# Performance work log

Hardware: AMD Instinct MI355X
Metric: run time of the kernel (lower is better)

The kernel has to match this reference:

```python
import jax, jax.numpy as jnp
import numpy as np
from jax import lax

ACT_BITS = 8
O, C, K = 256, 128, 3
STRIDE, PAD = 1, 1


def setup_inputs() -> dict:
    key = jax.random.key(0)
    kx, kw = jax.random.split(key)
    x = jax.random.uniform(kx, (16, C, 56, 56), dtype=jnp.float32)
    weight = jax.random.normal(kw, (O, C, K, K), dtype=jnp.float32)
    wrange = 2 ** 8  # weight_bits
    qw = jnp.clip(jnp.round(weight * (wrange - 1)), 0, wrange - 1)
    # PCILT: pcilt[o,c,kh,kw,i] = qw[o,c,kh,kw] * i  for i in [0, 2^act_bits)
    A = 2 ** ACT_BITS
    pcilt = qw[..., None] * jnp.arange(A, dtype=jnp.float32)  # [O,C,K,K,A]
    bias = jnp.zeros((O,), dtype=jnp.float32)
    return {"x": x, "pcilt": pcilt, "bias": bias}


def reference(x, pcilt, bias):
    A = pcilt.shape[-1]
    # quantize activations to integer LUT indices in [0, A-1]
    xq = jnp.clip(jnp.round(x * (A - 1)), 0.0, A - 1.0)
    # The gather-and-sum  out[b,o,h,w] = sum_{c,kh,kw} pcilt[o,c,kh,kw, idx]
    # is mathematically identical to a conv with qw = pcilt[...,1] applied to the
    # (float-cast) quantized indices, since pcilt[...,i] == qw * i exactly.
    qw = pcilt[..., 1]  # [O,C,K,K] quantized weights
    out = lax.conv_general_dilated(
        xq, qw,
        window_strides=(STRIDE, STRIDE),
        padding=((PAD, PAD), (PAD, PAD)),
        dimension_numbers=("NCHW", "OIHW", "NCHW"),
    )
    return out + bias[None, :, None, None]
```

## Files before the change

### kernel.cpp

```cpp
#include <hip/hip_runtime.h>
#include <stdint.h>

typedef unsigned short u16;
typedef __bf16 bf16x8 __attribute__((ext_vector_type(8)));
typedef float f32x4 __attribute__((ext_vector_type(4)));
typedef unsigned short u16x8 __attribute__((ext_vector_type(8)));

#define B_N   16
#define C_CH  128
#define O_CH  256
#define HW    56
#define PH    58
#define PW    72
#define PHW   (PH * PW)

__global__ void quant_pad(const float* __restrict__ x, u16* __restrict__ xp) {
    int idx = blockIdx.x * 256 + threadIdx.x;
    int wp = idx % PW;
    int hp = (idx / PW) % PH;
    int bc = idx / PHW;
    int h = hp - 1, w = wp - 1;
    u16 bits = 0;
    if ((unsigned)h < HW && (unsigned)w < HW) {
        float v = x[(bc * HW + h) * HW + w];
        float q = fminf(fmaxf(rintf(v * 255.0f), 0.0f), 255.0f);
        bits = (u16)(__float_as_uint(q) >> 16);
    }
    xp[idx] = bits;
}

__global__ void make_w(const float* __restrict__ pcilt, u16* __restrict__ Bq) {
    int idx = blockIdx.x * 256 + threadIdx.x;
    int o = idx % O_CH;
    int c = (idx / O_CH) % C_CH;
    int r = idx / (O_CH * C_CH);
    float v = pcilt[(size_t)(((o * C_CH + c) * 9 + r)) * 256 + 1];
    Bq[idx] = (u16)(__float_as_uint(v) >> 16);
}

__global__ __launch_bounds__(256) void conv_mfma(const u16* __restrict__ xp,
                                                 const u16* __restrict__ Bq,
                                                 const float* __restrict__ bias,
                                                 float* __restrict__ out) {
    __shared__ __align__(16) u16 Ws[4][128][8];
    __shared__ __align__(16) u16 Is[4][128][8];

    const int tid = threadIdx.x;
    const int o_blk = blockIdx.x * 128;
    const int h0 = blockIdx.y * 2;
    const int b = blockIdx.z;

    const int lane = tid & 63;
    const int wid = tid >> 6;
    const int wo = wid & 1;
    const int wm = wid >> 1;

    f32x4 acc[4][4];
#pragma unroll
    for (int i = 0; i < 4; i++)
#pragma unroll
        for (int j = 0; j < 4; j++) acc[i][j] = (f32x4){0.f, 0.f, 0.f, 0.f};

    const int sm = tid & 127;
    const int g0 = tid >> 7;
    const int sdh = sm >> 6;
    const int sw = sm & 63;

    const int quad = lane >> 4;
    const int lrow = lane & 15;

    for (int r = 0; r < 9; ++r) {
        const int kh = r / 3, kw = r % 3;
        const int xrow_base = (b * C_CH * PH + (h0 + sdh + kh)) * PW + (sw + kw);
        const int brow_base = r * C_CH * O_CH + (o_blk + sm);

        for (int cc = 0; cc < 4; ++cc) {
            const int c0 = cc * 32;
            __syncthreads();
#pragma unroll
            for (int gg = 0; gg < 2; ++gg) {
                const int g = g0 + gg * 2;
                u16x8 v;
#pragma unroll
                for (int e = 0; e < 8; ++e) {
                    const int c = c0 + g * 8 + e;
                    v[e] = xp[xrow_base + c * PHW];
                }
                *(u16x8*)&Is[g][sm][0] = v;
            }
#pragma unroll
            for (int gg = 0; gg < 2; ++gg) {
                const int g = g0 + gg * 2;
                u16x8 v;
#pragma unroll
                for (int e = 0; e < 8; ++e) {
                    const int c = c0 + g * 8 + e;
                    v[e] = Bq[brow_base + c * O_CH];
                }
                *(u16x8*)&Ws[g][sm][0] = v;
            }
            __syncthreads();
            bf16x8 af[4], bfr[4];
#pragma unroll
            for (int i = 0; i < 4; i++)
                af[i] = *(const bf16x8*)&Ws[quad][wo * 64 + i * 16 + lrow][0];
#pragma unroll
            for (int j = 0; j < 4; j++)
                bfr[j] = *(const bf16x8*)&Is[quad][wm * 64 + j * 16 + lrow][0];
#pragma unroll
            for (int i = 0; i < 4; i++)
#pragma unroll
                for (int j = 0; j < 4; j++)
                    acc[i][j] = __builtin_amdgcn_mfma_f32_16x16x32_bf16(af[i], bfr[j], acc[i][j], 0, 0, 0);
        }
    }

    const int hh = h0 + wm;
#pragma unroll
    for (int i = 0; i < 4; i++) {
        const int obase = o_blk + wo * 64 + i * 16 + quad * 4;
#pragma unroll
        for (int j = 0; j < 4; j++) {
            const int w = j * 16 + lrow;
            if (w < HW) {
#pragma unroll
                for (int rg = 0; rg < 4; ++rg) {
                    const int o = obase + rg;
                    out[(((size_t)b * O_CH + o) * HW + hh) * HW + w] = acc[i][j][rg] + bias[o];
                }
            }
        }
    }
}

extern "C" void kernel_launch(void* const* d_in, const int* in_sizes, int n_in,
                              void* d_out, int out_size, void* d_ws, size_t ws_size,
                              hipStream_t stream) {
    const float* x     = (const float*)d_in[0];
    const float* pcilt = (const float*)d_in[1];
    const float* bias  = (const float*)d_in[2];
    float* out = (float*)d_out;

    u16* xp = (u16*)d_ws;
    u16* Bq = xp + (size_t)B_N * C_CH * PHW;

    quant_pad<<<(B_N * C_CH * PHW) / 256, 256, 0, stream>>>(x, xp);
    make_w<<<(9 * C_CH * O_CH) / 256, 256, 0, stream>>>(pcilt, Bq);
    conv_mfma<<<dim3(O_CH / 128, HW / 2, B_N), dim3(256), 0, stream>>>(xp, Bq, bias, out);
}
```

Measured before the change: 453.5 us.

## Switch activations and weights to channel-last layout with direct global-to-LDS loads

The quantize/pad kernel now writes activations in NHWC order (channels innermost) through an LDS transpose, and the weight table is stored with input channel innermost. With contiguous channels, the conv kernel fills its LDS tiles with 16-byte global_load_lds transfers instead of eight strided 2-byte gathers per element. This removes uncoalesced scalar loads and register staging from the main loop. The cost is a more involved quantize kernel with a shared-memory transpose.

```diff
diff --git a/kernel.cpp b/kernel.cpp
--- a/kernel.cpp
+++ b/kernel.cpp
@@ -4,7 +4,6 @@
 typedef unsigned short u16;
 typedef __bf16 bf16x8 __attribute__((ext_vector_type(8)));
 typedef float f32x4 __attribute__((ext_vector_type(4)));
-typedef unsigned short u16x8 __attribute__((ext_vector_type(8)));
 
 #define B_N   16
 #define C_CH  128
@@ -12,28 +11,50 @@
 #define HW    56
 #define PH    58
 #define PW    72
-#define PHW   (PH * PW)
 
-__global__ void quant_pad(const float* __restrict__ x, u16* __restrict__ xp) {
-    int idx = blockIdx.x * 256 + threadIdx.x;
-    int wp = idx % PW;
-    int hp = (idx / PW) % PH;
-    int bc = idx / PHW;
-    int h = hp - 1, w = wp - 1;
-    u16 bits = 0;
-    if ((unsigned)h < HW && (unsigned)w < HW) {
-        float v = x[(bc * HW + h) * HW + w];
-        float q = fminf(fmaxf(rintf(v * 255.0f), 0.0f), 255.0f);
-        bits = (u16)(__float_as_uint(q) >> 16);
-    }
-    xp[idx] = bits;
+#define GLOBAL_AS __attribute__((address_space(1)))
+#define LDS_AS    __attribute__((address_space(3)))
+
+__device__ __forceinline__ void glds16(const u16* g, u16* l) {
+    __builtin_amdgcn_global_load_lds((const GLOBAL_AS void*)g, (LDS_AS void*)l, 16, 0, 0);
 }
 
-__global__ void make_w(const float* __restrict__ pcilt, u16* __restrict__ Bq) {
+__global__ __launch_bounds__(256) void quant_pad(const float* __restrict__ x,
+                                                 u16* __restrict__ xp) {
+    __shared__ u16 Lt[C_CH][58];
+    const int hp = blockIdx.x;
+    const int b = blockIdx.y;
+    const int tid = threadIdx.x;
+    const int h = hp - 1;
+    const bool interior = (unsigned)h < HW;
+
+    if (interior) {
+        for (int i = 0; i < 28; ++i) {
+            int idx = i * 256 + tid;
+            int c = idx / HW, w = idx % HW;
+            float v = x[((b * C_CH + c) * HW + h) * HW + w];
+            float q = fminf(fmaxf(rintf(v * 255.0f), 0.0f), 255.0f);
+            Lt[c][w] = (u16)(__float_as_uint(q) >> 16);
+        }
+    }
+    __syncthreads();
+    u16* dst = xp + ((size_t)(b * PH + hp) * PW) * C_CH;
+    for (int j = 0; j < 36; ++j) {
+        int idx = j * 256 + tid;
+        int wp = idx / C_CH, c = idx % C_CH;
+        int w = wp - 1;
+        u16 bits = 0;
+        if (interior && (unsigned)w < HW) bits = Lt[c][w];
+        dst[idx] = bits;
+    }
+}
+
+__global__ __launch_bounds__(256) void make_w(const float* __restrict__ pcilt,
+                                              u16* __restrict__ Bq) {
     int idx = blockIdx.x * 256 + threadIdx.x;
-    int o = idx % O_CH;
-    int c = (idx / O_CH) % C_CH;
-    int r = idx / (O_CH * C_CH);
+    int c = idx % C_CH;
+    int o = (idx / C_CH) % O_CH;
+    int r = idx / (C_CH * O_CH);
     float v = pcilt[(size_t)(((o * C_CH + c) * 9 + r)) * 256 + 1];
     Bq[idx] = (u16)(__float_as_uint(v) >> 16);
 }
@@ -61,45 +82,33 @@
 #pragma unroll
         for (int j = 0; j < 4; j++) acc[i][j] = (f32x4){0.f, 0.f, 0.f, 0.f};
 
-    const int sm = tid & 127;
-    const int g0 = tid >> 7;
-    const int sdh = sm >> 6;
-    const int sw = sm & 63;
+    const u16* pI0 = xp + ((size_t)(b * PH + h0) * PW + lane) * C_CH + wid * 8;
+    const u16* pI1 = pI0 + (size_t)PW * C_CH;
+    const u16* pW0 = Bq + (size_t)(o_blk + lane) * C_CH + wid * 8;
+    const u16* pW1 = pW0 + 64 * C_CH;
+    u16* lI0 = &Is[wid][0][0];
+    u16* lI1 = &Is[wid][64][0];
+    u16* lW0 = &Ws[wid][0][0];
+    u16* lW1 = &Ws[wid][64][0];
 
     const int quad = lane >> 4;
     const int lrow = lane & 15;
 
     for (int r = 0; r < 9; ++r) {
         const int kh = r / 3, kw = r % 3;
-        const int xrow_base = (b * C_CH * PH + (h0 + sdh + kh)) * PW + (sw + kw);
-        const int brow_base = r * C_CH * O_CH + (o_blk + sm);
+        const int offI_r = (kh * PW + kw) * C_CH;
+        const int offW_r = r * O_CH * C_CH;
+#pragma unroll
+        for (int cc = 0; cc < 4; ++cc) {
+            const int offI = offI_r + cc * 32;
+            const int offW = offW_r + cc * 32;
+            __syncthreads();
+            glds16(pI0 + offI, lI0);
+            glds16(pI1 + offI, lI1);
+            glds16(pW0 + offW, lW0);
+            glds16(pW1 + offW, lW1);
+            __syncthreads();
 
-        for (int cc = 0; cc < 4; ++cc) {
-            const int c0 = cc * 32;
-            __syncthreads();
-#pragma unroll
-            for (int gg = 0; gg < 2; ++gg) {
-                const int g = g0 + gg * 2;
-                u16x8 v;
-#pragma unroll
-                for (int e = 0; e < 8; ++e) {
-                    const int c = c0 + g * 8 + e;
-                    v[e] = xp[xrow_base + c * PHW];
-                }
-                *(u16x8*)&Is[g][sm][0] = v;
-            }
-#pragma unroll
-            for (int gg = 0; gg < 2; ++gg) {
-                const int g = g0 + gg * 2;
-                u16x8 v;
-#pragma unroll
-                for (int e = 0; e < 8; ++e) {
-                    const int c = c0 + g * 8 + e;
-                    v[e] = Bq[brow_base + c * O_CH];
-                }
-                *(u16x8*)&Ws[g][sm][0] = v;
-            }
-            __syncthreads();
             bf16x8 af[4], bfr[4];
 #pragma unroll
             for (int i = 0; i < 4; i++)
@@ -142,9 +151,9 @@
     float* out = (float*)d_out;
 
     u16* xp = (u16*)d_ws;
-    u16* Bq = xp + (size_t)B_N * C_CH * PHW;
+    u16* Bq = xp + (size_t)B_N * PH * PW * C_CH;
 
-    quant_pad<<<(B_N * C_CH * PHW) / 256, 256, 0, stream>>>(x, xp);
-    make_w<<<(9 * C_CH * O_CH) / 256, 256, 0, stream>>>(pcilt, Bq);
+    quant_pad<<<dim3(PH, B_N), 256, 0, stream>>>(x, xp);
+    make_w<<<(9 * O_CH * C_CH) / 256, 256, 0, stream>>>(pcilt, Bq);
     conv_mfma<<<dim3(O_CH / 128, HW / 2, B_N), dim3(256), 0, stream>>>(xp, Bq, bias, out);
 }
```

New measurement: 455.4 us. About the same (+0.4%).
